# Performance work log

Measured on AMD Instinct MI355X. Metric: run time of the kernel, lower is better.

The kernel has to match this reference:

```python
import jax, jax.numpy as jnp
import numpy as np

N = 32768        # total nodes (B * max_num_nodes)
E = 524288       # edges, avg degree 16
F_ORI = 32       # data.x_ori feature dim
F_G = 32         # each gamora_output feature dim
IN = F_ORI + 3 * F_G  # 128
H = 256          # hidden_dim
OUT = 16         # out_dim
MAXN = 1024      # max_num_nodes
EPS = 1e-5       # BatchNorm eps


def setup_inputs() -> dict:
    key = jax.random.key(0)
    ks = list(jax.random.split(key, 32))
    g = lambda k, shape, fan: jax.random.normal(k, shape, jnp.float32) / np.sqrt(fan)
    inp = {}
    inp['x_ori'] = jax.random.normal(ks[0], (N, F_ORI), jnp.float32)
    inp['g0'] = jax.random.normal(ks[1], (N, F_G), jnp.float32)
    inp['g1'] = jax.random.normal(ks[2], (N, F_G), jnp.float32)
    inp['g2'] = jax.random.normal(ks[3], (N, F_G), jnp.float32)
    inp['edge_index'] = jax.random.randint(ks[4], (2, E), 0, N, jnp.int64)
    # SAGEConv layer 0: in_dim -> hidden
    inp['Wl0'] = g(ks[5], (IN, H), IN)
    inp['Wr0'] = g(ks[6], (IN, H), IN)
    inp['bb0'] = jnp.zeros((H,), jnp.float32)
    # SAGEConv layers 1..3: hidden -> hidden (stacked)
    inp['Wl'] = g(ks[7], (3, H, H), H)
    inp['Wr'] = g(ks[8], (3, H, H), H)
    inp['bb'] = jnp.zeros((3, H), jnp.float32)
    # BatchNorm per conv layer
    inp['gamma'] = jnp.ones((4, H), jnp.float32)
    inp['beta'] = jnp.zeros((4, H), jnp.float32)
    # mlp1: [max_num_nodes, hidden, 1]
    inp['W1a'] = g(ks[9], (MAXN, H), MAXN)
    inp['b1a'] = jnp.zeros((H,), jnp.float32)
    inp['W1b'] = g(ks[10], (H, 1), H)
    inp['b1b'] = jnp.zeros((1,), jnp.float32)
    # final BatchNorm
    inp['gamma_f'] = jnp.ones((H,), jnp.float32)
    inp['beta_f'] = jnp.zeros((H,), jnp.float32)
    # mlp2: [hidden, hidden, out_dim]
    inp['W2a'] = g(ks[11], (H, H), H)
    inp['b2a'] = jnp.zeros((H,), jnp.float32)
    inp['W2b'] = g(ks[12], (H, OUT), H)
    inp['b2b'] = jnp.zeros((OUT,), jnp.float32)
    return inp


def _bn(x, gamma, beta):
    # training-mode BatchNorm1d over the node/batch axis (biased variance)
    m = jnp.mean(x, axis=0)
    v = jnp.var(x, axis=0)
    return (x - m) * jax.lax.rsqrt(v + EPS) * gamma + beta


def _sage(x, src, dst, inv_deg, Wl, Wr, b):
    # mean neighbor aggregation (gather -> segment_sum -> normalize), then
    # out = lin_l(mean_agg) + lin_r(x)  (PyG SAGEConv, aggr='mean')
    agg = jax.ops.segment_sum(x[src], dst, num_segments=N)
    mean = agg * inv_deg[:, None]
    return mean @ Wl + x @ Wr + b


def reference(x_ori, g0, g1, g2, edge_index, Wl0, Wr0, bb0, Wl, Wr, bb,
              gamma, beta, W1a, b1a, W1b, b1b, gamma_f, beta_f,
              W2a, b2a, W2b, b2b):
    x = jnp.concatenate([x_ori, g0, g1, g2], axis=1)  # [N, IN]
    dst, src = edge_index[0], edge_index[1]
    deg = jax.ops.segment_sum(jnp.ones((E,), x.dtype), dst, num_segments=N)
    inv_deg = jnp.where(deg > 0, 1.0 / jnp.maximum(deg, 1.0), 0.0)
    # layer 0
    x = jax.nn.relu(_bn(_sage(x, src, dst, inv_deg, Wl0, Wr0, bb0), gamma[0], beta[0]))
    # layers 1..3 (dropout is identity in eval-mode reference)
    for i in range(3):
        x = jax.nn.relu(_bn(_sage(x, src, dst, inv_deg, Wl[i], Wr[i], bb[i]),
                            gamma[i + 1], beta[i + 1]))
    x = x.reshape(-1, H, MAXN)                 # [B, H, MAXN]
    h = jax.nn.relu(x @ W1a + b1a)             # [B, H, H]
    x = (h @ W1b + b1b).squeeze(2)             # [B, H]
    x = jax.nn.relu(_bn(x, gamma_f, beta_f))
    x = jax.nn.relu(x @ W2a + b2a) @ W2b + b2b  # [B, OUT]
    return x
```

## Files before the change

### kernel.cpp

```cpp
#include <hip/hip_runtime.h>

#define NN 32768
#define NE 524288
#define HD 256
#define TOTP 794897

#define GAS __attribute__((address_space(1)))
#define LAS __attribute__((address_space(3)))

typedef __attribute__((ext_vector_type(8))) __bf16 bf16x8;
typedef __attribute__((ext_vector_type(4))) float f32x4;

__device__ __forceinline__ float ld_any(const void* p, int i, int isbf16) {
    return isbf16 ? (float)((const __bf16*)p)[i] : ((const float*)p)[i];
}

struct PtrTable { const void* p[18]; };


__global__ __launch_bounds__(256) void k_pre(const unsigned* __restrict__ xw, const int* __restrict__ ei,
                                             PtrTable pt, const void* __restrict__ p0, const void* __restrict__ p1,
                                             const void* __restrict__ p2, const void* __restrict__ p3,
                                             int* __restrict__ flags, int* __restrict__ deg,
                                             __bf16* __restrict__ blob, __bf16* __restrict__ X0c) {
    __shared__ int fl[2];
    const int t = threadIdx.x;
    if (t < 64) {
        unsigned L = xw[t] & 0xFFFFu;
        int e = (int)((L >> 7) & 0xFF);
        unsigned long long b = __ballot(e >= 90 && e <= 135);
        if (t == 0) fl[0] = (b == ~0ULL) ? 1 : 0;
    } else if (t < 128) {
        int u = t - 64;
        unsigned long long b = __ballot(ei[2 * u + 1] != 0);
        if (t == 64) fl[1] = (b == 0ULL) ? 1 : 0;
    }
    __syncthreads();
    const int f0 = fl[0], f1 = fl[1];
    const int blk = blockIdx.x;
    if (blk == 0 && t < 2) flags[t] = fl[t];
    if (blk < 2048) {
        int i0 = (blk * 256 + t) * 8;
        int n = i0 >> 7, f = i0 & 127;
        const void* src = (f < 32) ? p0 : (f < 64) ? p1 : (f < 96) ? p2 : p3;
        int si = n * 32 + (f & 31);
        bf16x8 o;
        #pragma unroll
        for (int j = 0; j < 8; ++j) o[j] = (__bf16)ld_any(src, si + j, f0);
        *(bf16x8*)&X0c[i0] = o;
    } else if (blk < 3601) {
        const int off[23] = {0, 32768, 65536, 65792, 131328, 196864, 262400, 327936, 393472,
                             459008, 459776, 460800, 461824, 723968, 724224, 724480, 724481,
                             724737, 724993, 790529, 790785, 794881, TOTP};
        const signed char pidx[22] = {0, 1, 2, 3, 3, 3, 4, 4, 4, 5, 6, 7, 8, 9, 10, 11, 12, 13, 14, 15, 16, 17};
        const int sbase[22] = {0, 0, 0, 0, 65536, 131072, 0, 65536, 131072, 0, 0, 0, 0, 0, 0, 0, 0, 0, 0, 0, 0, 0};
        const signed char lR[22] = {7, 7, -1, 8, 8, 8, 8, 8, 8, -1, -1, -1, 10, -1, -1, -1, -1, -1, -1, -1, -1, -1};
        const signed char lC[22] = {8, 8, 0, 8, 8, 8, 8, 8, 8, 0, 0, 0, 8, 0, 0, 0, 0, 0, 0, 0, 0, 0};
        int base = ((blk - 2048) * 256 + t) * 2;
        #pragma unroll
        for (int j = 0; j < 2; ++j) {
            int i = base + j;
            if (i >= TOTP) break;
            int s = 0;
            while (i >= off[s + 1]) ++s;
            int jj = i - off[s];
            int si;
            if (lR[s] >= 0) {
                int Rm = (1 << lR[s]) - 1;
                si = sbase[s] + ((jj & Rm) << lC[s]) + (jj >> lR[s]);
            } else {
                si = sbase[s] + jj;
            }
            blob[i] = (__bf16)ld_any(pt.p[pidx[s]], si, f0);
        }
    } else {
        int e0 = ((blk - 3601) * 256 + t) * 2;
        int d0 = f1 ? ei[2 * e0] : ei[e0];
        int d1 = f1 ? ei[2 * e0 + 2] : ei[e0 + 1];
        atomicAdd(&deg[d0], 1);
        atomicAdd(&deg[d1], 1);
    }
}


__global__ __launch_bounds__(256) void k_alloc(const int* __restrict__ deg, int* __restrict__ gcur,
                                               int* __restrict__ offs, float* __restrict__ invd) {
    const int n = blockIdx.x * 256 + threadIdx.x;
    const int lane = threadIdx.x & 63;
    const int v = deg[n];
    invd[n] = v ? 1.f / (float)v : 0.f;
    int incl = v;
    #pragma unroll
    for (int d = 1; d < 64; d <<= 1) {
        int y = __shfl_up(incl, d, 64);
        if (lane >= d) incl += y;
    }
    int base = 0;
    if (lane == 63) base = atomicAdd(gcur, incl);
    base = __shfl(base, 63, 64);
    offs[n] = base + incl - v;
}

__global__ __launch_bounds__(256) void k_fill(const int* __restrict__ ei, const int* __restrict__ flags,
                                              const int* __restrict__ offs, int* __restrict__ cursor,
                                              int* __restrict__ csr) {
    int e = blockIdx.x * 256 + threadIdx.x;
    int f = flags[1];
    int d = f ? ei[2 * e] : ei[e];
    int s = f ? ei[2 * NE + 2 * e] : ei[NE + e];
    int p = atomicAdd(&cursor[d], 1);
    csr[offs[d] + p] = s;
}


__global__ __launch_bounds__(256) void k_agg0(const __bf16* __restrict__ X, const int* __restrict__ csr,
                                              const int* __restrict__ offs, const int* __restrict__ deg,
                                              const float* __restrict__ invd, __bf16* __restrict__ M) {
    const int t = threadIdx.x;
    const int s = blockIdx.x & 1;
    const int n = (blockIdx.x >> 1) * 32 + (t >> 3);
    const int fo = s * 64 + (t & 7) * 8;
    const int beg = offs[n], end = beg + deg[n];
    float a[8] = {};
    for (int e = beg; e < end; e += 8) {
        #pragma unroll
        for (int u = 0; u < 8; ++u) {
            int ee = e + u;
            int idx = csr[ee < end ? ee : end - 1] & (NN - 1);
            float mk = ee < end ? 1.f : 0.f;
            bf16x8 v = *(const bf16x8*)&X[(size_t)idx * 128 + fo];
            #pragma unroll
            for (int j = 0; j < 8; ++j) a[j] += mk * (float)v[j];
        }
    }
    const float id = invd[n];
    bf16x8 o;
    #pragma unroll
    for (int j = 0; j < 8; ++j) o[j] = (__bf16)(a[j] * id);
    *(bf16x8*)&M[(size_t)n * 128 + fo] = o;
}

__global__ __launch_bounds__(256) void k_agg(const __bf16* __restrict__ X, const int* __restrict__ csr,
                                             const int* __restrict__ offs, const int* __restrict__ deg,
                                             const float* __restrict__ invd, __bf16* __restrict__ M) {
    const int t = threadIdx.x;
    const int s = blockIdx.x & 3;
    const int n = (blockIdx.x >> 2) * 32 + (t >> 3);
    const int fo = s * 64 + (t & 7) * 8;
    const int beg = offs[n], end = beg + deg[n];
    float a[8] = {};
    for (int e = beg; e < end; e += 8) {
        #pragma unroll
        for (int u = 0; u < 8; ++u) {
            int ee = e + u;
            int idx = csr[ee < end ? ee : end - 1] & (NN - 1);
            float mk = ee < end ? 1.f : 0.f;
            bf16x8 v = *(const bf16x8*)&X[(size_t)idx * HD + fo];
            #pragma unroll
            for (int j = 0; j < 8; ++j) a[j] += mk * (float)v[j];
        }
    }
    const float id = invd[n];
    bf16x8 o;
    #pragma unroll
    for (int j = 0; j < 8; ++j) o[j] = (__bf16)(a[j] * id);
    *(bf16x8*)&M[(size_t)n * HD + fo] = o;
}


template <int MODE, int TM>
__global__ __launch_bounds__(256) void k_gemm(const __bf16* __restrict__ A1, const __bf16* __restrict__ WT1,
                                              const __bf16* __restrict__ A2, const __bf16* __restrict__ WT2,
                                              const __bf16* __restrict__ bias, int KD,
                                              __bf16* __restrict__ O, float* __restrict__ colsum,
                                              const __bf16* __restrict__ W1b, float* __restrict__ x2) {
    constexpr int MI = TM / 32;
    __shared__ __bf16 As[2][TM][32];
    __shared__ __bf16 Bs[2][128][32];
    const int t = threadIdx.x;
    const int lane = t & 63, w = t >> 6;
    const int wm = w >> 1, wn = w & 1;
    const int quad = lane >> 4, l15 = lane & 15;
    const int row0 = blockIdx.x * TM, c0 = blockIdx.y * 128;
    const int dr = lane >> 2, dc = (lane & 3) * 8;
    f32x4 acc[MI][4] = {};
    const int npass = A2 ? 2 : 1;
    for (int pass = 0; pass < npass; ++pass) {
        const __bf16* __restrict__ A = pass ? A2 : A1;
        const __bf16* __restrict__ WT = pass ? WT2 : WT1;
        for (int k0 = 0; k0 < KD; k0 += 64) {
            __syncthreads();
            #pragma unroll
            for (int kk = 0; kk < 2; ++kk) {
                #pragma unroll
                for (int i = 0; i < 2; ++i) {
                    const __bf16* g = &WT[(size_t)(c0 + w * 32 + i * 16 + dr) * KD + k0 + kk * 32 + dc];
                    __builtin_amdgcn_global_load_lds((const GAS void*)g, (LAS void*)&Bs[kk][w * 32 + i * 16][0],
                                                     16, 0, 0);
                }
                #pragma unroll
                for (int i = 0; i < TM / 64; ++i) {
                    const __bf16* g = &A[(size_t)(row0 + w * (TM / 4) + i * 16 + dr) * KD + k0 + kk * 32 + dc];
                    __builtin_amdgcn_global_load_lds((const GAS void*)g,
                                                     (LAS void*)&As[kk][w * (TM / 4) + i * 16][0], 16, 0, 0);
                }
            }
            __syncthreads();
            #pragma unroll
            for (int kk = 0; kk < 2; ++kk) {
                bf16x8 af[MI], bfr[4];
                #pragma unroll
                for (int i = 0; i < MI; ++i) af[i] = *(const bf16x8*)&As[kk][wm * (TM / 2) + i * 16 + l15][quad * 8];
                #pragma unroll
                for (int j = 0; j < 4; ++j) bfr[j] = *(const bf16x8*)&Bs[kk][wn * 64 + j * 16 + l15][quad * 8];
                #pragma unroll
                for (int i = 0; i < MI; ++i)
                    #pragma unroll
                    for (int j = 0; j < 4; ++j)
                        acc[i][j] = __builtin_amdgcn_mfma_f32_16x16x32_bf16(af[i], bfr[j], acc[i][j], 0, 0, 0);
            }
        }
    }
    __syncthreads();
    if constexpr (MODE == 0) {
        float* lsum = (float*)&As[0][0][0];
        lsum[t] = 0.f;
        __syncthreads();
        #pragma unroll
        for (int j = 0; j < 4; ++j) {
            const int cb = wn * 64 + j * 16 + l15;
            const int col = c0 + cb;
            const float b = (float)bias[col];
            float s = 0.f, q = 0.f;
            #pragma unroll
            for (int i = 0; i < MI; ++i) {
                const size_t rbase = (size_t)(row0 + wm * (TM / 2) + i * 16 + quad * 4) * HD + col;
                #pragma unroll
                for (int r = 0; r < 4; ++r) {
                    float y = acc[i][j][r] + b;
                    O[rbase + (size_t)r * HD] = (__bf16)y;
                    s += y;
                    q += y * y;
                }
            }
            s += __shfl_xor(s, 16, 64); s += __shfl_xor(s, 32, 64);
            q += __shfl_xor(q, 16, 64); q += __shfl_xor(q, 32, 64);
            if (quad == 0) {
                atomicAdd(&lsum[cb], s);
                atomicAdd(&lsum[128 + cb], q);
            }
        }
        __syncthreads();
        if (t < 128) atomicAdd(&colsum[c0 + t], lsum[t]);
        else atomicAdd(&colsum[256 + c0 + t - 128], lsum[t]);
    } else {
        float bj[4], wj[4];
        #pragma unroll
        for (int j = 0; j < 4; ++j) {
            const int col = c0 + wn * 64 + j * 16 + l15;
            bj[j] = (float)bias[col];
            wj[j] = (float)W1b[col];
        }
        #pragma unroll
        for (int i = 0; i < MI; ++i) {
            #pragma unroll
            for (int r = 0; r < 4; ++r) {
                float p = 0.f;
                #pragma unroll
                for (int j = 0; j < 4; ++j) p += fmaxf(acc[i][j][r] + bj[j], 0.f) * wj[j];
                p += __shfl_xor(p, 1, 64); p += __shfl_xor(p, 2, 64);
                p += __shfl_xor(p, 4, 64); p += __shfl_xor(p, 8, 64);
                if (l15 == 0) atomicAdd(&x2[row0 + wm * (TM / 2) + i * 16 + quad * 4 + r], p);
            }
        }
    }
}


__global__ __launch_bounds__(256) void k_bnapply(__bf16* __restrict__ Y, const float* __restrict__ pstat,
                                                 const __bf16* __restrict__ gamma, const __bf16* __restrict__ beta) {
    __shared__ float sc[256], sh[256];
    const int t = threadIdx.x;
    {
        const float invn = 1.0f / NN;
        float m = pstat[t] * invn;
        float var = fmaxf(pstat[256 + t] * invn - m * m, 0.f);
        float rs = rsqrtf(var + 1e-5f);
        float s = (float)gamma[t] * rs;
        sc[t] = s;
        sh[t] = (float)beta[t] - m * s;
    }
    __syncthreads();
    size_t i = ((size_t)blockIdx.x * 256 + t) * 8;
    int c = (int)(i & 255);
    bf16x8 y = *(const bf16x8*)&Y[i];
    bf16x8 o;
    #pragma unroll
    for (int j = 0; j < 8; ++j) o[j] = (__bf16)fmaxf((float)y[j] * sc[c + j] + sh[c + j], 0.f);
    *(bf16x8*)&Y[i] = o;
}


__global__ __launch_bounds__(256) void k_mlp2(const float* __restrict__ x2, const __bf16* __restrict__ b1b,
                                              const __bf16* __restrict__ gf, const __bf16* __restrict__ bf_,
                                              const __bf16* __restrict__ W2a, const __bf16* __restrict__ b2a,
                                              const __bf16* __restrict__ W2b, const __bf16* __restrict__ b2b,
                                              const int* __restrict__ flags, void* __restrict__ out) {
    __shared__ float row[HD];
    __shared__ float hbuf[HD];
    __shared__ float part[256];
    const int b = blockIdx.x, t = threadIdx.x;
    const float b1 = (float)b1b[0];
    float s = 0.f, q = 0.f, mine = 0.f;
    #pragma unroll
    for (int r = 0; r < 32; ++r) {
        float v = x2[r * HD + t] + b1;
        s += v; q += v * v;
        if (r == b) mine = v;
    }
    float m = s * (1.0f / 32.0f);
    float var = fmaxf(q * (1.0f / 32.0f) - m * m, 0.f);
    float rs = rsqrtf(var + 1e-5f);
    float sc = (float)gf[t] * rs;
    float sh = (float)bf_[t] - m * sc;
    row[t] = fmaxf(mine * sc + sh, 0.f);
    __syncthreads();
    float acc = (float)b2a[t];
    for (int j = 0; j < HD; ++j) acc += row[j] * (float)W2a[j * HD + t];
    hbuf[t] = fmaxf(acc, 0.f);
    __syncthreads();
    const int k = t & 15, g = t >> 4;
    float p = 0.f;
    #pragma unroll
    for (int jj = 0; jj < 16; ++jj) p += hbuf[g * 16 + jj] * (float)W2b[(g * 16 + jj) * 16 + k];
    part[t] = p;
    __syncthreads();
    if (t < 16) {
        float o = (float)b2b[t];
        #pragma unroll
        for (int g2 = 0; g2 < 16; ++g2) o += part[g2 * 16 + t];
        if (flags[0]) ((__bf16*)out)[b * 16 + t] = (__bf16)o;
        else ((float*)out)[b * 16 + t] = o;
    }
}


extern "C" void kernel_launch(void* const* d_in, const int* in_sizes, int n_in,
                              void* d_out, int out_size, void* d_ws, size_t ws_size,
                              hipStream_t stream) {
    const int* ei = (const int*)d_in[4];

    char* ws = (char*)d_ws;
    size_t off_ = 0;
    auto ALLOC = [&](size_t b) { char* p = ws + off_; off_ += (b + 255) & ~(size_t)255; return p; };
    int* flags_ = (int*)ALLOC(8);
    size_t zbeg = off_;
    int* deg_ = (int*)ALLOC(NN * 4);
    int* cursor_ = (int*)ALLOC(NN * 4);
    float* colsum_ = (float*)ALLOC(4 * 512 * 4);
    float* x2_ = (float*)ALLOC(8192 * 4);
    int* gcur_ = (int*)ALLOC(4);
    size_t zlen = off_ - zbeg;
    int* offs_ = (int*)ALLOC(NN * 4);
    float* invd_ = (float*)ALLOC(NN * 4);
    int* csr_ = (int*)ALLOC((size_t)NE * 4);
    __bf16* blob_ = (__bf16*)ALLOC((size_t)TOTP * 2);
    __bf16* M_ = (__bf16*)ALLOC((size_t)NN * HD * 2);
    __bf16* Xa_ = (__bf16*)ALLOC((size_t)NN * HD * 2);
    __bf16* Xb_ = (__bf16*)ALLOC((size_t)NN * HD * 2);
    __bf16* X0c_ = Xb_;

    __bf16* Wl0T = blob_ + 0;
    __bf16* Wr0T = blob_ + 32768;
    __bf16* bb0c = blob_ + 65536;
    __bf16* WlT = blob_ + 65792;
    __bf16* WrT = blob_ + 262400;
    __bf16* bbc = blob_ + 459008;
    __bf16* gammac = blob_ + 459776;
    __bf16* betac = blob_ + 460800;
    __bf16* W1aT = blob_ + 461824;
    __bf16* b1ac = blob_ + 723968;
    __bf16* W1bc = blob_ + 724224;
    __bf16* b1bc = blob_ + 724480;
    __bf16* gfc = blob_ + 724481;
    __bf16* bfc = blob_ + 724737;
    __bf16* W2ac = blob_ + 724993;
    __bf16* b2ac = blob_ + 790529;
    __bf16* W2bc = blob_ + 790785;
    __bf16* b2bc = blob_ + 794881;

    PtrTable pt;
    pt.p[0] = d_in[5];  pt.p[1] = d_in[6];  pt.p[2] = d_in[7];  pt.p[3] = d_in[8];
    pt.p[4] = d_in[9];  pt.p[5] = d_in[10]; pt.p[6] = d_in[11]; pt.p[7] = d_in[12];
    pt.p[8] = d_in[13]; pt.p[9] = d_in[14]; pt.p[10] = d_in[15]; pt.p[11] = d_in[16];
    pt.p[12] = d_in[17]; pt.p[13] = d_in[18]; pt.p[14] = d_in[19]; pt.p[15] = d_in[20];
    pt.p[16] = d_in[21]; pt.p[17] = d_in[22];

    hipMemsetAsync(ws + zbeg, 0, zlen, stream);
    k_pre<<<4625, 256, 0, stream>>>((const unsigned*)d_in[0], ei, pt, d_in[0], d_in[1], d_in[2], d_in[3],
                                    flags_, deg_, blob_, X0c_);
    k_alloc<<<NN / 256, 256, 0, stream>>>(deg_, gcur_, offs_, invd_);
    k_fill<<<NE / 256, 256, 0, stream>>>(ei, flags_, offs_, cursor_, csr_);

    k_agg0<<<NN / 32 * 2, 256, 0, stream>>>(X0c_, csr_, offs_, deg_, invd_, M_);
    k_gemm<0, 128><<<dim3(NN / 128, 2), 256, 0, stream>>>(M_, Wl0T, X0c_, Wr0T, bb0c, 128, Xa_, colsum_,
                                                          nullptr, nullptr);
    k_bnapply<<<NN / 8, 256, 0, stream>>>(Xa_, colsum_, gammac, betac);

    __bf16* Xin = Xa_;
    __bf16* Xo = Xb_;
    for (int l = 0; l < 3; ++l) {
        float* cs = colsum_ + (l + 1) * 512;
        k_agg<<<NN / 32 * 4, 256, 0, stream>>>(Xin, csr_, offs_, deg_, invd_, M_);
        k_gemm<0, 128><<<dim3(NN / 128, 2), 256, 0, stream>>>(M_, WlT + (size_t)l * HD * HD, Xin,
                                                              WrT + (size_t)l * HD * HD, bbc + l * HD, 256, Xo,
                                                              cs, nullptr, nullptr);
        k_bnapply<<<NN / 8, 256, 0, stream>>>(Xo, cs, gammac + (l + 1) * HD, betac + (l + 1) * HD);
        __bf16* tmp = Xin; Xin = Xo; Xo = tmp;
    }

    k_gemm<1, 64><<<dim3(8192 / 64, 2), 256, 0, stream>>>(Xin, W1aT, nullptr, nullptr, b1ac, 1024, nullptr,
                                                          nullptr, W1bc, x2_);
    k_mlp2<<<32, 256, 0, stream>>>(x2_, b1bc, gfc, bfc, W2ac, b2ac, W2bc, b2bc, flags_, d_out);
}
```

Before: 418.0 us.

## Fuse BatchNorm+ReLU apply into the next layer's aggregation and GEMM A-loads

Result: slower. 442.3 us (+5.8%).

```diff
diff --git a/kernel.cpp b/kernel.cpp
--- a/kernel.cpp
+++ b/kernel.cpp
@@ -140,13 +140,30 @@
     *(bf16x8*)&M[(size_t)n * 128 + fo] = o;
 }
 
-__global__ __launch_bounds__(256) void k_agg(const __bf16* __restrict__ X, const int* __restrict__ csr,
-                                             const int* __restrict__ offs, const int* __restrict__ deg,
-                                             const float* __restrict__ invd, __bf16* __restrict__ M) {
+
+__global__ __launch_bounds__(256) void k_aggbn(const __bf16* __restrict__ X, const int* __restrict__ csr,
+                                               const int* __restrict__ offs, const int* __restrict__ deg,
+                                               const float* __restrict__ invd, const float* __restrict__ pstat,
+                                               const __bf16* __restrict__ gamma, const __bf16* __restrict__ beta,
+                                               __bf16* __restrict__ M) {
     const int t = threadIdx.x;
     const int s = blockIdx.x & 3;
     const int n = (blockIdx.x >> 2) * 32 + (t >> 3);
     const int fo = s * 64 + (t & 7) * 8;
+    float sc[8], sh[8];
+    {
+        const float invn = 1.0f / NN;
+        #pragma unroll
+        for (int j = 0; j < 8; ++j) {
+            const int c = fo + j;
+            float m = pstat[c] * invn;
+            float var = fmaxf(pstat[256 + c] * invn - m * m, 0.f);
+            float rs = rsqrtf(var + 1e-5f);
+            float g = (float)gamma[c] * rs;
+            sc[j] = g;
+            sh[j] = (float)beta[c] - m * g;
+        }
+    }
     const int beg = offs[n], end = beg + deg[n];
     float a[8] = {};
     for (int e = beg; e < end; e += 8) {
@@ -157,7 +174,7 @@
             float mk = ee < end ? 1.f : 0.f;
             bf16x8 v = *(const bf16x8*)&X[(size_t)idx * HD + fo];
             #pragma unroll
-            for (int j = 0; j < 8; ++j) a[j] += mk * (float)v[j];
+            for (int j = 0; j < 8; ++j) a[j] += mk * fmaxf((float)v[j] * sc[j] + sh[j], 0.f);
         }
     }
     const float id = invd[n];
@@ -168,21 +185,33 @@
 }
 
 
-template <int MODE, int TM>
+template <int MODE, int TM, int BNA>
 __global__ __launch_bounds__(256) void k_gemm(const __bf16* __restrict__ A1, const __bf16* __restrict__ WT1,
                                               const __bf16* __restrict__ A2, const __bf16* __restrict__ WT2,
                                               const __bf16* __restrict__ bias, int KD,
                                               __bf16* __restrict__ O, float* __restrict__ colsum,
-                                              const __bf16* __restrict__ W1b, float* __restrict__ x2) {
+                                              const __bf16* __restrict__ W1b, float* __restrict__ x2,
+                                              const float* __restrict__ pstatA, const __bf16* __restrict__ gA,
+                                              const __bf16* __restrict__ bA) {
     constexpr int MI = TM / 32;
     __shared__ __bf16 As[2][TM][32];
     __shared__ __bf16 Bs[2][128][32];
+    __shared__ float scs[256], shs[256];
     const int t = threadIdx.x;
     const int lane = t & 63, w = t >> 6;
     const int wm = w >> 1, wn = w & 1;
     const int quad = lane >> 4, l15 = lane & 15;
     const int row0 = blockIdx.x * TM, c0 = blockIdx.y * 128;
     const int dr = lane >> 2, dc = (lane & 3) * 8;
+    if constexpr (BNA != 0) {
+        const float invn = 1.0f / NN;
+        float m = pstatA[t] * invn;
+        float var = fmaxf(pstatA[256 + t] * invn - m * m, 0.f);
+        float rs = rsqrtf(var + 1e-5f);
+        float g = (float)gA[t] * rs;
+        scs[t] = g;
+        shs[t] = (float)bA[t] - m * g;
+    }
     f32x4 acc[MI][4] = {};
     const int npass = A2 ? 2 : 1;
     for (int pass = 0; pass < npass; ++pass) {
@@ -198,11 +227,25 @@
                     __builtin_amdgcn_global_load_lds((const GAS void*)g, (LAS void*)&Bs[kk][w * 32 + i * 16][0],
                                                      16, 0, 0);
                 }
-                #pragma unroll
-                for (int i = 0; i < TM / 64; ++i) {
-                    const __bf16* g = &A[(size_t)(row0 + w * (TM / 4) + i * 16 + dr) * KD + k0 + kk * 32 + dc];
-                    __builtin_amdgcn_global_load_lds((const GAS void*)g,
-                                                     (LAS void*)&As[kk][w * (TM / 4) + i * 16][0], 16, 0, 0);
+                if ((BNA >> pass) & 1) {
+                    const int kb = (k0 + kk * 32 + dc) & 255;
+                    #pragma unroll
+                    for (int i = 0; i < TM / 64; ++i) {
+                        const __bf16* g = &A[(size_t)(row0 + w * (TM / 4) + i * 16 + dr) * KD + k0 + kk * 32 + dc];
+                        bf16x8 v = *(const bf16x8*)g;
+                        bf16x8 o;
+                        #pragma unroll
+                        for (int j = 0; j < 8; ++j)
+                            o[j] = (__bf16)fmaxf((float)v[j] * scs[kb + j] + shs[kb + j], 0.f);
+                        *(bf16x8*)&As[kk][w * (TM / 4) + i * 16 + dr][dc] = o;
+                    }
+                } else {
+                    #pragma unroll
+                    for (int i = 0; i < TM / 64; ++i) {
+                        const __bf16* g = &A[(size_t)(row0 + w * (TM / 4) + i * 16 + dr) * KD + k0 + kk * 32 + dc];
+                        __builtin_amdgcn_global_load_lds((const GAS void*)g,
+                                                         (LAS void*)&As[kk][w * (TM / 4) + i * 16 + dr][0], 16, 0, 0);
+                    }
                 }
             }
             __syncthreads();
@@ -274,30 +317,6 @@
             }
         }
     }
-}
-
-
-__global__ __launch_bounds__(256) void k_bnapply(__bf16* __restrict__ Y, const float* __restrict__ pstat,
-                                                 const __bf16* __restrict__ gamma, const __bf16* __restrict__ beta) {
-    __shared__ float sc[256], sh[256];
-    const int t = threadIdx.x;
-    {
-        const float invn = 1.0f / NN;
-        float m = pstat[t] * invn;
-        float var = fmaxf(pstat[256 + t] * invn - m * m, 0.f);
-        float rs = rsqrtf(var + 1e-5f);
-        float s = (float)gamma[t] * rs;
-        sc[t] = s;
-        sh[t] = (float)beta[t] - m * s;
-    }
-    __syncthreads();
-    size_t i = ((size_t)blockIdx.x * 256 + t) * 8;
-    int c = (int)(i & 255);
-    bf16x8 y = *(const bf16x8*)&Y[i];
-    bf16x8 o;
-    #pragma unroll
-    for (int j = 0; j < 8; ++j) o[j] = (__bf16)fmaxf((float)y[j] * sc[c + j] + sh[c + j], 0.f);
-    *(bf16x8*)&Y[i] = o;
 }
 
 
@@ -403,23 +422,25 @@
     k_fill<<<NE / 256, 256, 0, stream>>>(ei, flags_, offs_, cursor_, csr_);
 
     k_agg0<<<NN / 32 * 2, 256, 0, stream>>>(X0c_, csr_, offs_, deg_, invd_, M_);
-    k_gemm<0, 128><<<dim3(NN / 128, 2), 256, 0, stream>>>(M_, Wl0T, X0c_, Wr0T, bb0c, 128, Xa_, colsum_,
-                                                          nullptr, nullptr);
-    k_bnapply<<<NN / 8, 256, 0, stream>>>(Xa_, colsum_, gammac, betac);
+    k_gemm<0, 128, 0><<<dim3(NN / 128, 2), 256, 0, stream>>>(M_, Wl0T, X0c_, Wr0T, bb0c, 128, Xa_, colsum_,
+                                                             nullptr, nullptr, nullptr, nullptr, nullptr);
 
     __bf16* Xin = Xa_;
     __bf16* Xo = Xb_;
     for (int l = 0; l < 3; ++l) {
+        float* csprev = colsum_ + l * 512;
         float* cs = colsum_ + (l + 1) * 512;
-        k_agg<<<NN / 32 * 4, 256, 0, stream>>>(Xin, csr_, offs_, deg_, invd_, M_);
-        k_gemm<0, 128><<<dim3(NN / 128, 2), 256, 0, stream>>>(M_, WlT + (size_t)l * HD * HD, Xin,
-                                                              WrT + (size_t)l * HD * HD, bbc + l * HD, 256, Xo,
-                                                              cs, nullptr, nullptr);
-        k_bnapply<<<NN / 8, 256, 0, stream>>>(Xo, cs, gammac + (l + 1) * HD, betac + (l + 1) * HD);
+        k_aggbn<<<NN / 32 * 4, 256, 0, stream>>>(Xin, csr_, offs_, deg_, invd_, csprev,
+                                                 gammac + l * HD, betac + l * HD, M_);
+        k_gemm<0, 128, 2><<<dim3(NN / 128, 2), 256, 0, stream>>>(M_, WlT + (size_t)l * HD * HD, Xin,
+                                                                 WrT + (size_t)l * HD * HD, bbc + l * HD, 256, Xo,
+                                                                 cs, nullptr, nullptr, csprev,
+                                                                 gammac + l * HD, betac + l * HD);
         __bf16* tmp = Xin; Xin = Xo; Xo = tmp;
     }
 
-    k_gemm<1, 64><<<dim3(8192 / 64, 2), 256, 0, stream>>>(Xin, W1aT, nullptr, nullptr, b1ac, 1024, nullptr,
-                                                          nullptr, W1bc, x2_);
+    k_gemm<1, 64, 1><<<dim3(8192 / 64, 2), 256, 0, stream>>>(Xin, W1aT, nullptr, nullptr, b1ac, 1024, nullptr,
+                                                             nullptr, W1bc, x2_, colsum_ + 3 * 512,
+                                                             gammac + 3 * HD, betac + 3 * HD);
     k_mlp2<<<32, 256, 0, stream>>>(x2_, b1bc, gfc, bfc, W2ac, b2ac, W2bc, b2bc, flags_, d_out);
 }
```
